# Kernel tuning notes

Measured on AMD Instinct MI355X. Metric: run time of the kernel, lower is better.

The kernel has to match this reference:

```python
import jax, jax.numpy as jnp
import numpy as np

N_ENT, N_USR, C, E, NNZ, NREL, NHOPS = 150000, 60000, 64, 1000000, 1000000, 10, 2
EPS = 1e-12  # torch F.normalize default eps


def setup_inputs() -> dict:
    key = jax.random.key(0)
    ks = jax.random.split(key, 8)
    return {
        "user_emb": jax.random.normal(ks[0], (N_USR, C), dtype=jnp.float32),
        "entity_emb": jax.random.normal(ks[1], (N_ENT, C), dtype=jnp.float32),
        "weight": jax.random.normal(ks[2], (NREL - 1, C), dtype=jnp.float32) * 0.1,  # xavier-ish
        "inter_vals": jax.random.uniform(ks[3], (NNZ,), dtype=jnp.float32),
        "edge_index": jax.random.randint(ks[4], (2, E), 0, N_ENT),
        "edge_type": jax.random.randint(ks[5], (E,), 0, NREL - 1),
        "inter_rows": jax.random.randint(ks[6], (NNZ,), 0, N_USR),
        "inter_cols": jax.random.randint(ks[7], (NNZ,), 0, N_ENT),
    }


def _l2_normalize(x):
    n = jnp.sqrt(jnp.sum(x * x, axis=1, keepdims=True))
    return x / jnp.maximum(n, EPS)


def _hop(entity_emb, user_emb, head, tail, edge_type, weight,
         inter_rows, inter_cols, inter_vals):
    rel = weight[edge_type - 1]                      # [E, C]
    h = entity_emb[head]                             # [E, C]
    t = entity_emb[tail]                             # [E, C]
    neigh = t * rel                                  # [E, C]
    # calculate_sim_hrt: (||h*r||_2 * ||t*r||_2)^2, per-edge scalar
    hn = jnp.linalg.norm(h * rel, axis=1)            # [E]
    tn = jnp.linalg.norm(t * rel, axis=1)            # [E]
    att = (hn * tn) ** 2                             # [E]
    # scatter_softmax over groups of `head` (value identical across channels)
    m = jax.ops.segment_max(att, head, num_segments=N_ENT)
    e = jnp.exp(att - m[head])
    s = jax.ops.segment_sum(e, head, num_segments=N_ENT)
    w = e / s[head]                                  # [E]
    entity_agg = jax.ops.segment_sum(w[:, None] * neigh, head, num_segments=N_ENT)
    # entity_agg += interact_mat.T @ user_emb
    entity_agg = entity_agg + jax.ops.segment_sum(
        inter_vals[:, None] * user_emb[inter_rows], inter_cols, num_segments=N_ENT)
    # user_agg = interact_mat @ entity_emb
    user_agg = jax.ops.segment_sum(
        inter_vals[:, None] * entity_emb[inter_cols], inter_rows, num_segments=N_USR)
    return entity_agg, user_agg


def reference(user_emb, entity_emb, weight, inter_vals,
              edge_index, edge_type, inter_rows, inter_cols):
    head, tail = edge_index[0], edge_index[1]
    ent_res, usr_res = entity_emb, user_emb
    ent, usr = entity_emb, user_emb
    for _ in range(NHOPS):
        ent, usr = _hop(ent, usr, head, tail, edge_type, weight,
                        inter_rows, inter_cols, inter_vals)
        ent = _l2_normalize(ent)  # mess_dropout disabled (eval path)
        usr = _l2_normalize(usr)
        ent_res = ent_res + ent
        usr_res = usr_res + usr
    return ent_res, usr_res
```

## Files before the change

### kernel.cpp

```cpp
#include <hip/hip_runtime.h>
#include <hip/hip_fp16.h>
#include <math.h>

#define N_ENT  150000
#define N_USR  60000
#define CDIM   64
#define NE     1000000
#define NNZV   1000000
#define NREL9  9
#define NTOT   (2 * N_ENT + N_USR)
#define TOTAL_ITEMS (NE + 2 * NNZV)
#define SCAN_B ((NTOT + 1023) / 1024)

#define NXCD   8
#define H_PER  (N_ENT / NXCD)
#define R_PER  (N_USR / NXCD)
#define EPB    2048
#define NCHUNK ((NE + EPB - 1) / EPB)

#define EG (N_ENT / 4)
#define UG (N_USR / 4)
#define UCVT ((N_USR * CDIM / 2 + 255) / 256)

template <int CTRL>
__device__ __forceinline__ float dpp_addf(float v) {
    int iv = __float_as_int(v);
    int x = __builtin_amdgcn_update_dpp(iv, iv, CTRL, 0xF, 0xF, true);
    return v + __int_as_float(x);
}
template <int CTRL>
__device__ __forceinline__ float dpp_maxf(float v) {
    int iv = __float_as_int(v);
    int x = __builtin_amdgcn_update_dpp(iv, iv, CTRL, 0xF, 0xF, true);
    return fmaxf(v, __int_as_float(x));
}
__device__ __forceinline__ float wave_sum(float v) {
    v = dpp_addf<0x111>(v);
    v = dpp_addf<0x112>(v);
    v = dpp_addf<0x114>(v);
    v = dpp_addf<0x118>(v);
    v = dpp_addf<0x142>(v);
    v = dpp_addf<0x143>(v);
    return __int_as_float(__builtin_amdgcn_readlane(__float_as_int(v), 63));
}
__device__ __forceinline__ float wave_max(float v) {
    v = dpp_maxf<0x111>(v);
    v = dpp_maxf<0x112>(v);
    v = dpp_maxf<0x114>(v);
    v = dpp_maxf<0x118>(v);
    v = dpp_maxf<0x142>(v);
    v = dpp_maxf<0x143>(v);
    return __int_as_float(__builtin_amdgcn_readlane(__float_as_int(v), 63));
}

__device__ __forceinline__ int   bcast_i(int v, int l)   { return __builtin_amdgcn_readlane(v, l); }
__device__ __forceinline__ float bcast_f(float v, int l) { return __int_as_float(__builtin_amdgcn_readlane(__float_as_int(v), l)); }

__device__ __forceinline__ int block_excl_scan(int v, int* lds) {
    int lane = threadIdx.x & 63, wid = threadIdx.x >> 6;
    int incl = v;
#pragma unroll
    for (int o = 1; o < 64; o <<= 1) {
        int t = __shfl_up(incl, o, 64);
        if (lane >= o) incl += t;
    }
    if (lane == 63) lds[wid] = incl;
    __syncthreads();
    int nw = blockDim.x >> 6;
    if ((int)threadIdx.x < nw) {
        int s = lds[threadIdx.x];
        int si = s;
        for (int o = 1; o < nw; o <<= 1) {
            int t = __shfl_up(si, o, 64);
            if ((int)threadIdx.x >= o) si += t;
        }
        lds[threadIdx.x] = si - s;
    }
    __syncthreads();
    return incl - v + lds[wid];
}

__global__ __launch_bounds__(256) void k_zero(int* __restrict__ p, int n) {
    int i = blockIdx.x * 256 + threadIdx.x;
    if (i < n) p[i] = 0;
}


__global__ __launch_bounds__(256) void k_hist(
    const int* __restrict__ head, const int* __restrict__ cols,
    const int* __restrict__ rows, int* __restrict__ cnt)
{
    int role  = blockIdx.x & (NXCD - 1);
    int chunk = blockIdx.x >> 3;
    int h0 = role * H_PER, h1 = h0 + H_PER;
    int r0 = role * R_PER, r1 = r0 + R_PER;
    int base = chunk * EPB;
    int end  = min(base + EPB, NE);
    for (int i = base + (int)threadIdx.x; i < end; i += 256) {
        int h = head[i];
        int c = cols[i];
        int r = rows[i];
        if (h >= h0 && h < h1) atomicAdd(cnt + h, 1);
        if (c >= h0 && c < h1) atomicAdd(cnt + N_ENT + c, 1);
        if (r >= r0 && r < r1) atomicAdd(cnt + 2 * N_ENT + r, 1);
    }
}

__global__ __launch_bounds__(1024) void k_bsum(
    const int* __restrict__ cnt, int* __restrict__ bsum)
{
    __shared__ int lds[16];
    int i = blockIdx.x * 1024 + threadIdx.x;
    float v = (i < NTOT) ? (float)cnt[i] : 0.f;
    float s = wave_sum(v);
    int lane = threadIdx.x & 63, wid = threadIdx.x >> 6;
    if (lane == 0) lds[wid] = (int)s;
    __syncthreads();
    if (threadIdx.x == 0) {
        int t = 0;
        for (int k = 0; k < 16; ++k) t += lds[k];
        bsum[blockIdx.x] = t;
    }
}

__global__ __launch_bounds__(512) void k_scan_small(int* __restrict__ bsum)
{
    __shared__ int lds[16];
    int i = threadIdx.x;
    int v = (i < SCAN_B) ? bsum[i] : 0;
    int e = block_excl_scan(v, lds);
    if (i < SCAN_B) bsum[i] = e;
}

__global__ __launch_bounds__(1024) void k_scan_apply(
    const int* __restrict__ cnt, const int* __restrict__ bsum,
    int* __restrict__ start, int* __restrict__ cursor)
{
    __shared__ int lds[16];
    int i = blockIdx.x * 1024 + threadIdx.x;
    int v = (i < NTOT) ? cnt[i] : 0;
    int e = block_excl_scan(v, lds) + bsum[blockIdx.x];
    if (i < NTOT) { start[i] = e; cursor[i] = e; }
    else if (i == NTOT) { start[i] = TOTAL_ITEMS; }
}

__global__ __launch_bounds__(256) void k_scatter(
    const int* __restrict__ head, const int* __restrict__ tail,
    const int* __restrict__ etype,
    const int* __restrict__ rows, const int* __restrict__ cols,
    const float* __restrict__ vals,
    int* __restrict__ cursor,
    int* __restrict__ pk_h,
    int2* __restrict__ rc,
    int2* __restrict__ cv)
{
    int role  = blockIdx.x & (NXCD - 1);
    int chunk = blockIdx.x >> 3;
    int h0 = role * H_PER, h1 = h0 + H_PER;
    int r0 = role * R_PER, r1 = r0 + R_PER;
    int base = chunk * EPB;
    int end  = min(base + EPB, NE);
    for (int i = base + (int)threadIdx.x; i < end; i += 256) {
        int h = head[i];
        int c = cols[i];
        int r = rows[i];
        if (h >= h0 && h < h1) {
            int rt = etype[i] - 1;
            if (rt < 0) rt = 8;
            int p = atomicAdd(cursor + h, 1);
            if ((unsigned)p < (unsigned)NE) pk_h[p] = tail[i] | (rt << 18);
        }
        if (c >= h0 && c < h1) {
            int vb = __float_as_int(vals[i]);
            int p = atomicAdd(cursor + N_ENT + c, 1) - NE;
            if ((unsigned)p < (unsigned)NNZV) rc[p] = make_int2(r, vb);
        }
        if (r >= r0 && r < r1) {
            int vb = __float_as_int(vals[i]);
            int p = atomicAdd(cursor + 2 * N_ENT + r, 1) - 2 * NE;
            if ((unsigned)p < (unsigned)NNZV) cv[p] = make_int2(c, vb);
        }
    }
}

__global__ __launch_bounds__(256) void k_prep(
    const float* __restrict__ ent, const float* __restrict__ usr,
    const float* __restrict__ wt,
    __half* __restrict__ ent16, __half* __restrict__ usr16,
    float* __restrict__ sq)
{
    int b = blockIdx.x;
    if (b < EG) {
        int e = (b * 256 + (int)threadIdx.x) >> 6;
        int lane = threadIdx.x & 63;
        float own = ent[(e << 6) + lane];
        ent16[(e << 6) + lane] = __float2half(own);
        float o2 = own * own;
        float mine = 0.f;
#pragma unroll
        for (int rt = 0; rt < NREL9; ++rt) {
            float r = wt[(rt << 6) + lane];
            float s = wave_sum(o2 * r * r);
            if (lane == rt) mine = s;
        }
        if (lane < NREL9) sq[e * NREL9 + lane] = mine;
    } else {
        int i = (b - EG) * 256 + (int)threadIdx.x;
        if (i < N_USR * CDIM / 2) {
            float2 v = ((const float2*)usr)[i];
            ((__half2*)usr16)[i] = __floats2half2_rn(v.x, v.y);
        }
    }
}

template <bool FIRST, bool LAST>
__global__ __launch_bounds__(256) void k_hop(
    const __half* __restrict__ ent16_cur, const __half* __restrict__ usr16_cur,
    const float* __restrict__ ent_res_base, const float* __restrict__ usr_res_base,
    const float* __restrict__ wt, const int* __restrict__ start,
    const int* __restrict__ pk_h, const float* __restrict__ sq_in,
    const int2* __restrict__ rc, const int2* __restrict__ cv,
    __half* __restrict__ ent16_next, __half* __restrict__ usr16_next,
    float* __restrict__ sq_out,
    float* __restrict__ out_ent, float* __restrict__ out_usr)
{
    int lane = threadIdx.x & 63;
    int b = blockIdx.x;

    if (b < EG) {
        int e = (b * 256 + (int)threadIdx.x) >> 6;

        int s1 = min(start[e + 1], NE);
        int s0 = min(start[e], s1);
        float m = 0.f, l = 0.f, acc = 0.f;
        for (int base = s0; base < s1; base += 64) {
            int j = base + lane;
            int cnt = min(64, s1 - base);
            int pk = 0; float att = 0.f;
            if (j < s1) {
                pk = pk_h[j];
                int t = pk & 0x3FFFF, rt = (pk >> 18) & 15;
                att = sq_in[e * NREL9 + rt] * sq_in[t * NREL9 + rt];
            }
            float mn = fmaxf(m, wave_max(att));
            float scale = __expf(m - mn);
            float p = (j < s1) ? __expf(att - mn) : 0.f;
            l = l * scale + wave_sum(p);
            acc *= scale;
            m = mn;
            int k = 0;
            for (; k + 4 <= cnt; k += 4) {
#pragma unroll
                for (int q = 0; q < 4; ++q) {
                    int pkk = bcast_i(pk, k + q);
                    float wk = bcast_f(p, k + q);
                    const __half* tp = ent16_cur + ((pkk & 0x3FFFF) << 6);
                    const float*  wp = wt + (((pkk >> 18) & 15) << 6);
                    acc += wk * __half2float(tp[lane]) * wp[lane];
                }
            }
            for (; k < cnt; ++k) {
                int pkk = bcast_i(pk, k);
                float wk = bcast_f(p, k);
                const __half* tp = ent16_cur + ((pkk & 0x3FFFF) << 6);
                const float*  wp = wt + (((pkk >> 18) & 15) << 6);
                acc += wk * __half2float(tp[lane]) * wp[lane];
            }
        }
        float agg = (l > 0.f) ? acc / l : 0.f;

        int c1 = min(start[N_ENT + e + 1] - NE, NNZV);
        int c0 = max(min(start[N_ENT + e] - NE, c1), 0);
        for (int base = c0; base < c1; base += 64) {
            int j = base + lane;
            int cnt = min(64, c1 - base);
            int rr = 0; float vv = 0.f;
            if (j < c1) { int2 q = rc[j]; rr = q.x; vv = __int_as_float(q.y); }
            int k = 0;
            for (; k + 4 <= cnt; k += 4) {
#pragma unroll
                for (int q = 0; q < 4; ++q) {
                    int u = bcast_i(rr, k + q);
                    float v = bcast_f(vv, k + q);
                    agg += v * __half2float(usr16_cur[(u << 6) + lane]);
                }
            }
            for (; k < cnt; ++k) {
                int u = bcast_i(rr, k);
                float v = bcast_f(vv, k);
                agg += v * __half2float(usr16_cur[(u << 6) + lane]);
            }
        }

        float s = wave_sum(agg * agg);
        float y = agg / fmaxf(sqrtf(s), 1e-12f);
        int oi = (e << 6) + lane;
        if (!LAST) {
            ent16_next[oi] = __float2half(y);
            float y2 = y * y;
            float mine = 0.f;
#pragma unroll
            for (int rt = 0; rt < NREL9; ++rt) {
                float r = wt[(rt << 6) + lane];
                float sv = wave_sum(y2 * r * r);
                if (lane == rt) mine = sv;
            }
            if (lane < NREL9) sq_out[e * NREL9 + lane] = mine;
        }
        if (FIRST) out_ent[oi] = ent_res_base[oi] + y;
        else       out_ent[oi] += y;
    } else {
        int u = ((b - EG) * 256 + (int)threadIdx.x) >> 6;
        int s1 = min(start[2 * N_ENT + u + 1] - 2 * NE, NNZV);
        int s0 = max(min(start[2 * N_ENT + u] - 2 * NE, s1), 0);
        float acc = 0.f;
        for (int base = s0; base < s1; base += 64) {
            int j = base + lane;
            int cnt = min(64, s1 - base);
            int cc = 0; float vv = 0.f;
            if (j < s1) { int2 q = cv[j]; cc = q.x; vv = __int_as_float(q.y); }
            int k = 0;
            for (; k + 4 <= cnt; k += 4) {
#pragma unroll
                for (int q = 0; q < 4; ++q) {
                    int c = bcast_i(cc, k + q);
                    float v = bcast_f(vv, k + q);
                    acc += v * __half2float(ent16_cur[(c << 6) + lane]);
                }
            }
            for (; k < cnt; ++k) {
                int c = bcast_i(cc, k);
                float v = bcast_f(vv, k);
                acc += v * __half2float(ent16_cur[(c << 6) + lane]);
            }
        }
        float s = wave_sum(acc * acc);
        float y = acc / fmaxf(sqrtf(s), 1e-12f);
        int oi = (u << 6) + lane;
        if (!LAST) usr16_next[oi] = __float2half(y);
        if (FIRST) out_usr[oi] = usr_res_base[oi] + y;
        else       out_usr[oi] += y;
    }
}

extern "C" void kernel_launch(void* const* d_in, const int* in_sizes, int n_in,
                              void* d_out, int out_size, void* d_ws, size_t ws_size,
                              hipStream_t stream)
{
    const float* user_emb   = (const float*)d_in[0];
    const float* entity_emb = (const float*)d_in[1];
    const float* wt         = (const float*)d_in[2];
    const float* inter_vals = (const float*)d_in[3];
    const int*   edge_index = (const int*)d_in[4];
    const int*   etype      = (const int*)d_in[5];
    const int*   inter_rows = (const int*)d_in[6];
    const int*   inter_cols = (const int*)d_in[7];
    const int* head  = edge_index;
    const int* tailp = edge_index + NE;

    __half* ent16_a = (__half*)d_ws;
    __half* ent16_b = ent16_a + (size_t)N_ENT * CDIM;
    __half* usr16_a = ent16_b + (size_t)N_ENT * CDIM;
    __half* usr16_b = usr16_a + (size_t)N_USR * CDIM;
    int2*  rc     = (int2*)(usr16_b + (size_t)N_USR * CDIM);
    int2*  cv     = rc + NNZV;
    int*   pk_h   = (int*)(cv + NNZV);
    int*   cnt    = pk_h + NE;
    int*   start  = cnt + NTOT;
    int*   cursor = start + NTOT + 1;
    int*   bsum   = cursor + NTOT + 1;
    float* sq_a   = (float*)(bsum + SCAN_B);
    float* sq_b   = sq_a + (size_t)N_ENT * NREL9;

    float* out_ent = (float*)d_out;
    float* out_usr = out_ent + (size_t)N_ENT * CDIM;

    k_zero<<<(NTOT + 255) / 256, 256, 0, stream>>>(cnt, NTOT);
    k_hist<<<NCHUNK * NXCD, 256, 0, stream>>>(head, inter_cols, inter_rows, cnt);
    k_bsum<<<SCAN_B, 1024, 0, stream>>>(cnt, bsum);
    k_scan_small<<<1, 512, 0, stream>>>(bsum);
    k_scan_apply<<<SCAN_B, 1024, 0, stream>>>(cnt, bsum, start, cursor);
    k_scatter<<<NCHUNK * NXCD, 256, 0, stream>>>(
        head, tailp, etype, inter_rows, inter_cols, inter_vals,
        cursor, pk_h, rc, cv);

    k_prep<<<EG + UCVT, 256, 0, stream>>>(
        entity_emb, user_emb, wt, ent16_a, usr16_a, sq_a);

    k_hop<true, false><<<EG + UG, 256, 0, stream>>>(
        ent16_a, usr16_a, entity_emb, user_emb, wt, start, pk_h, sq_a, rc, cv,
        ent16_b, usr16_b, sq_b, out_ent, out_usr);

    k_hop<false, true><<<EG + UG, 256, 0, stream>>>(
        ent16_b, usr16_b, nullptr, nullptr, wt, start, pk_h, sq_b, rc, cv,
        nullptr, nullptr, nullptr, out_ent, out_usr);
}
```

Measured before the change: 700.8 us.

## Fuse histogram with embedding prep and unroll gathers by eight with dual accumulators

Merges the histogram kernel and the fp16/sq prep kernel into a single launch, and swaps the zeroing kernel for hipMemsetAsync. This removes one launch and lets the independent prep work overlap the atomic histogram. The gather loops in k_hop are unrolled by 8 with predicated tails and two alternating accumulators, so more loads are in flight and the FMA dependency chain is shorter. In exchange, short segments do masked-off gather iterations that still issue redundant loads, and register pressure rises.

New measurement: 708.7 us. Within noise of the previous version (+1.1%).

```diff
diff --git a/kernel.cpp b/kernel.cpp
--- a/kernel.cpp
+++ b/kernel.cpp
@@ -17,6 +17,7 @@
 #define R_PER  (N_USR / NXCD)
 #define EPB    2048
 #define NCHUNK ((NE + EPB - 1) / EPB)
+#define HISTB  (NCHUNK * NXCD)
 
 #define EG (N_ENT / 4)
 #define UG (N_USR / 4)
@@ -80,29 +81,50 @@
     return incl - v + lds[wid];
 }
 
-__global__ __launch_bounds__(256) void k_zero(int* __restrict__ p, int n) {
-    int i = blockIdx.x * 256 + threadIdx.x;
-    if (i < n) p[i] = 0;
-}
-
-
-__global__ __launch_bounds__(256) void k_hist(
+__global__ __launch_bounds__(256) void k_histprep(
     const int* __restrict__ head, const int* __restrict__ cols,
-    const int* __restrict__ rows, int* __restrict__ cnt)
-{
-    int role  = blockIdx.x & (NXCD - 1);
-    int chunk = blockIdx.x >> 3;
-    int h0 = role * H_PER, h1 = h0 + H_PER;
-    int r0 = role * R_PER, r1 = r0 + R_PER;
-    int base = chunk * EPB;
-    int end  = min(base + EPB, NE);
-    for (int i = base + (int)threadIdx.x; i < end; i += 256) {
-        int h = head[i];
-        int c = cols[i];
-        int r = rows[i];
-        if (h >= h0 && h < h1) atomicAdd(cnt + h, 1);
-        if (c >= h0 && c < h1) atomicAdd(cnt + N_ENT + c, 1);
-        if (r >= r0 && r < r1) atomicAdd(cnt + 2 * N_ENT + r, 1);
+    const int* __restrict__ rows, int* __restrict__ cnt,
+    const float* __restrict__ ent, const float* __restrict__ usr,
+    const float* __restrict__ wt,
+    __half* __restrict__ ent16, __half* __restrict__ usr16,
+    float* __restrict__ sq)
+{
+    int b = blockIdx.x;
+    if (b < HISTB) {
+        int role  = b & (NXCD - 1);
+        int chunk = b >> 3;
+        int h0 = role * H_PER, h1 = h0 + H_PER;
+        int r0 = role * R_PER, r1 = r0 + R_PER;
+        int base = chunk * EPB;
+        int end  = min(base + EPB, NE);
+        for (int i = base + (int)threadIdx.x; i < end; i += 256) {
+            int h = head[i];
+            int c = cols[i];
+            int r = rows[i];
+            if (h >= h0 && h < h1) atomicAdd(cnt + h, 1);
+            if (c >= h0 && c < h1) atomicAdd(cnt + N_ENT + c, 1);
+            if (r >= r0 && r < r1) atomicAdd(cnt + 2 * N_ENT + r, 1);
+        }
+    } else if (b < HISTB + EG) {
+        int e = ((b - HISTB) * 256 + (int)threadIdx.x) >> 6;
+        int lane = threadIdx.x & 63;
+        float own = ent[(e << 6) + lane];
+        ent16[(e << 6) + lane] = __float2half(own);
+        float o2 = own * own;
+        float mine = 0.f;
+#pragma unroll
+        for (int rt = 0; rt < NREL9; ++rt) {
+            float r = wt[(rt << 6) + lane];
+            float s = wave_sum(o2 * r * r);
+            if (lane == rt) mine = s;
+        }
+        if (lane < NREL9) sq[e * NREL9 + lane] = mine;
+    } else {
+        int i = (b - HISTB - EG) * 256 + (int)threadIdx.x;
+        if (i < N_USR * CDIM / 2) {
+            float2 v = ((const float2*)usr)[i];
+            ((__half2*)usr16)[i] = __floats2half2_rn(v.x, v.y);
+        }
     }
 }
 
@@ -183,36 +205,6 @@
     }
 }
 
-__global__ __launch_bounds__(256) void k_prep(
-    const float* __restrict__ ent, const float* __restrict__ usr,
-    const float* __restrict__ wt,
-    __half* __restrict__ ent16, __half* __restrict__ usr16,
-    float* __restrict__ sq)
-{
-    int b = blockIdx.x;
-    if (b < EG) {
-        int e = (b * 256 + (int)threadIdx.x) >> 6;
-        int lane = threadIdx.x & 63;
-        float own = ent[(e << 6) + lane];
-        ent16[(e << 6) + lane] = __float2half(own);
-        float o2 = own * own;
-        float mine = 0.f;
-#pragma unroll
-        for (int rt = 0; rt < NREL9; ++rt) {
-            float r = wt[(rt << 6) + lane];
-            float s = wave_sum(o2 * r * r);
-            if (lane == rt) mine = s;
-        }
-        if (lane < NREL9) sq[e * NREL9 + lane] = mine;
-    } else {
-        int i = (b - EG) * 256 + (int)threadIdx.x;
-        if (i < N_USR * CDIM / 2) {
-            float2 v = ((const float2*)usr)[i];
-            ((__half2*)usr16)[i] = __floats2half2_rn(v.x, v.y);
-        }
-    }
-}
-
 template <bool FIRST, bool LAST>
 __global__ __launch_bounds__(256) void k_hop(
     const __half* __restrict__ ent16_cur, const __half* __restrict__ usr16_cur,
@@ -232,7 +224,8 @@
 
         int s1 = min(start[e + 1], NE);
         int s0 = min(start[e], s1);
-        float m = 0.f, l = 0.f, acc = 0.f;
+        float m = 0.f, l = 0.f;
+        float accA = 0.f, accB = 0.f;
         for (int base = s0; base < s1; base += 64) {
             int j = base + lane;
             int cnt = min(64, s1 - base);
@@ -246,51 +239,46 @@
             float scale = __expf(m - mn);
             float p = (j < s1) ? __expf(att - mn) : 0.f;
             l = l * scale + wave_sum(p);
-            acc *= scale;
+            accA *= scale; accB *= scale;
             m = mn;
-            int k = 0;
-            for (; k + 4 <= cnt; k += 4) {
-#pragma unroll
-                for (int q = 0; q < 4; ++q) {
-                    int pkk = bcast_i(pk, k + q);
-                    float wk = bcast_f(p, k + q);
+            for (int k = 0; k < cnt; k += 8) {
+#pragma unroll
+                for (int q = 0; q < 8; ++q) {
+                    int kk = k + q;
+                    int sel = (kk < cnt) ? kk : 0;
+                    int pkk = bcast_i(pk, sel);
+                    float wk = (kk < cnt) ? bcast_f(p, sel) : 0.f;
                     const __half* tp = ent16_cur + ((pkk & 0x3FFFF) << 6);
                     const float*  wp = wt + (((pkk >> 18) & 15) << 6);
-                    acc += wk * __half2float(tp[lane]) * wp[lane];
+                    float prod = wk * __half2float(tp[lane]) * wp[lane];
+                    if (q & 1) accB += prod; else accA += prod;
                 }
             }
-            for (; k < cnt; ++k) {
-                int pkk = bcast_i(pk, k);
-                float wk = bcast_f(p, k);
-                const __half* tp = ent16_cur + ((pkk & 0x3FFFF) << 6);
-                const float*  wp = wt + (((pkk >> 18) & 15) << 6);
-                acc += wk * __half2float(tp[lane]) * wp[lane];
-            }
-        }
+        }
+        float acc = accA + accB;
         float agg = (l > 0.f) ? acc / l : 0.f;
 
         int c1 = min(start[N_ENT + e + 1] - NE, NNZV);
         int c0 = max(min(start[N_ENT + e] - NE, c1), 0);
+        float agA = 0.f, agB = 0.f;
         for (int base = c0; base < c1; base += 64) {
             int j = base + lane;
             int cnt = min(64, c1 - base);
             int rr = 0; float vv = 0.f;
             if (j < c1) { int2 q = rc[j]; rr = q.x; vv = __int_as_float(q.y); }
-            int k = 0;
-            for (; k + 4 <= cnt; k += 4) {
-#pragma unroll
-                for (int q = 0; q < 4; ++q) {
-                    int u = bcast_i(rr, k + q);
-                    float v = bcast_f(vv, k + q);
-                    agg += v * __half2float(usr16_cur[(u << 6) + lane]);
+            for (int k = 0; k < cnt; k += 8) {
+#pragma unroll
+                for (int q = 0; q < 8; ++q) {
+                    int kk = k + q;
+                    int sel = (kk < cnt) ? kk : 0;
+                    int u = bcast_i(rr, sel);
+                    float v = (kk < cnt) ? bcast_f(vv, sel) : 0.f;
+                    float prod = v * __half2float(usr16_cur[(u << 6) + lane]);
+                    if (q & 1) agB += prod; else agA += prod;
                 }
             }
-            for (; k < cnt; ++k) {
-                int u = bcast_i(rr, k);
-                float v = bcast_f(vv, k);
-                agg += v * __half2float(usr16_cur[(u << 6) + lane]);
-            }
-        }
+        }
+        agg += agA + agB;
 
         float s = wave_sum(agg * agg);
         float y = agg / fmaxf(sqrtf(s), 1e-12f);
@@ -313,27 +301,25 @@
         int u = ((b - EG) * 256 + (int)threadIdx.x) >> 6;
         int s1 = min(start[2 * N_ENT + u + 1] - 2 * NE, NNZV);
         int s0 = max(min(start[2 * N_ENT + u] - 2 * NE, s1), 0);
-        float acc = 0.f;
+        float acA = 0.f, acB = 0.f;
         for (int base = s0; base < s1; base += 64) {
             int j = base + lane;
             int cnt = min(64, s1 - base);
             int cc = 0; float vv = 0.f;
             if (j < s1) { int2 q = cv[j]; cc = q.x; vv = __int_as_float(q.y); }
-            int k = 0;
-            for (; k + 4 <= cnt; k += 4) {
-#pragma unroll
-                for (int q = 0; q < 4; ++q) {
-                    int c = bcast_i(cc, k + q);
-                    float v = bcast_f(vv, k + q);
-                    acc += v * __half2float(ent16_cur[(c << 6) + lane]);
+            for (int k = 0; k < cnt; k += 8) {
+#pragma unroll
+                for (int q = 0; q < 8; ++q) {
+                    int kk = k + q;
+                    int sel = (kk < cnt) ? kk : 0;
+                    int c = bcast_i(cc, sel);
+                    float v = (kk < cnt) ? bcast_f(vv, sel) : 0.f;
+                    float prod = v * __half2float(ent16_cur[(c << 6) + lane]);
+                    if (q & 1) acB += prod; else acA += prod;
                 }
             }
-            for (; k < cnt; ++k) {
-                int c = bcast_i(cc, k);
-                float v = bcast_f(vv, k);
-                acc += v * __half2float(ent16_cur[(c << 6) + lane]);
-            }
-        }
+        }
+        float acc = acA + acB;
         float s = wave_sum(acc * acc);
         float y = acc / fmaxf(sqrtf(s), 1e-12f);
         int oi = (u << 6) + lane;
@@ -375,8 +361,10 @@
     float* out_ent = (float*)d_out;
     float* out_usr = out_ent + (size_t)N_ENT * CDIM;
 
-    k_zero<<<(NTOT + 255) / 256, 256, 0, stream>>>(cnt, NTOT);
-    k_hist<<<NCHUNK * NXCD, 256, 0, stream>>>(head, inter_cols, inter_rows, cnt);
+    hipMemsetAsync(cnt, 0, (size_t)NTOT * sizeof(int), stream);
+    k_histprep<<<HISTB + EG + UCVT, 256, 0, stream>>>(
+        head, inter_cols, inter_rows, cnt,
+        entity_emb, user_emb, wt, ent16_a, usr16_a, sq_a);
     k_bsum<<<SCAN_B, 1024, 0, stream>>>(cnt, bsum);
     k_scan_small<<<1, 512, 0, stream>>>(bsum);
     k_scan_apply<<<SCAN_B, 1024, 0, stream>>>(cnt, bsum, start, cursor);
@@ -384,9 +372,6 @@
         head, tailp, etype, inter_rows, inter_cols, inter_vals,
         cursor, pk_h, rc, cv);
 
-    k_prep<<<EG + UCVT, 256, 0, stream>>>(
-        entity_emb, user_emb, wt, ent16_a, usr16_a, sq_a);
-
     k_hop<true, false><<<EG + UG, 256, 0, stream>>>(
         ent16_a, usr16_a, entity_emb, user_emb, wt, start, pk_h, sq_a, rc, cv,
         ent16_b, usr16_b, sq_b, out_ent, out_usr);
```
